# Performance work log

Measured on AMD Instinct MI355X. Metric: run time of the kernel, lower is better.

## Reference

```python
import jax, jax.numpy as jnp
import numpy as np

NC, ND, B, K = 10000, 1000000, 8192, 64
EMB = 16
CH_DENSE, DEV_DENSE = 16, 20
CAT_MAX = [100, 4, 50, 200, 500, 1000, 300]  # lang, plat, os, country, carrier, brand, plat_os
H1, H2, ATTN_H = 64, 64, 84
IN1 = CH_DENSE + EMB        # 32  (channel dense + channel_id emb)
IN2 = DEV_DENSE + 7 * EMB   # 132 (device dense + 7 cat embs)


def setup_inputs() -> dict:
    key = jax.random.key(0)
    ks = jax.random.split(key, 32)
    def nrm(k, shape, s=0.05):
        return jax.random.normal(k, shape, dtype=jnp.float32) * s
    inp = {}
    inp["channel_dense"] = nrm(ks[0], (NC, CH_DENSE), 1.0)
    inp["device_dense"] = nrm(ks[1], (ND, DEV_DENSE), 1.0)
    inp["channel_id_emb"] = nrm(ks[2], (NC, EMB))
    names = ["lang_emb", "plat_emb", "os_emb", "country_emb", "carrier_emb", "brand_emb", "plat_os_emb"]
    for i, (n, m) in enumerate(zip(names, CAT_MAX)):
        inp[n] = nrm(ks[3 + i], (m, EMB))
    inp["W_agg"] = nrm(ks[10], (IN2, H2));  inp["b_agg"] = jnp.zeros((H2,), jnp.float32)
    inp["W_self"] = nrm(ks[11], (IN1, H1)); inp["b_self"] = jnp.zeros((H1,), jnp.float32)
    inp["W_attn"] = nrm(ks[12], (H2 + IN1, ATTN_H)); inp["b_attn"] = jnp.zeros((ATTN_H,), jnp.float32)
    inp["W_attn2"] = nrm(ks[13], (ATTN_H, 1)); inp["b_attn2"] = jnp.zeros((1,), jnp.float32)
    inp["channel_ids"] = jax.random.randint(ks[14], (NC,), 0, NC)
    cat_cols = [jax.random.randint(ks[15 + i], (ND,), 0, m) for i, m in enumerate(CAT_MAX)]
    inp["device_cat"] = jnp.stack(cat_cols, axis=1)  # [ND, 7]
    inp["vertices"] = jax.random.randint(ks[22], (B,), 0, NC)
    inp["bot_neibrs"] = jax.random.randint(ks[23], (B, K), 0, ND)
    inp["normal_neibrs"] = jax.random.randint(ks[24], (B, K), 0, ND)
    inp["bot_counts"] = jax.random.randint(ks[25], (B,), 1, K + 1)
    inp["normal_counts"] = jax.random.randint(ks[26], (B,), 1, K + 1)
    return inp


def reference(channel_dense, device_dense, channel_id_emb, lang_emb, plat_emb, os_emb,
              country_emb, carrier_emb, brand_emb, plat_os_emb,
              W_agg, b_agg, W_self, b_self, W_attn, b_attn, W_attn2, b_attn2,
              channel_ids, device_cat, vertices, bot_neibrs, normal_neibrs,
              bot_counts, normal_counts):
    cat_tables = [lang_emb, plat_emb, os_emb, country_emb, carrier_emb, brand_emb, plat_os_emb]
    # channel self features: dense cols + channel_id embedding  -> [B, IN1]
    ch_v = jnp.concatenate([channel_dense[vertices],
                            channel_id_emb[channel_ids[vertices]]], axis=1)

    def agg(neibrs, counts):
        # gather neighbor device features, embed categoricals, masked mean, linear (Mean_agg)
        dense = device_dense[neibrs]                                   # [B, K, DEV_DENSE]
        cats = device_cat[neibrs]                                      # [B, K, 7]
        embs = jnp.concatenate([t[cats[..., i]] for i, t in enumerate(cat_tables)], axis=-1)
        feats = jnp.concatenate([dense, embs], axis=-1)                # [B, K, IN2]
        mask = (jnp.arange(K)[None, :] < counts[:, None]).astype(feats.dtype)
        mean = jnp.sum(feats * mask[..., None], axis=1) / jnp.maximum(counts, 1).astype(feats.dtype)[:, None]
        return mean @ W_agg + b_agg                                    # [B, H2]

    bots = agg(bot_neibrs, bot_counts)
    normal = agg(normal_neibrs, normal_counts)

    def score(h):
        # attention MLP on concat(aggregated feats, channel self feats)
        return jax.nn.relu(jnp.concatenate([h, ch_v], axis=1) @ W_attn + b_attn) @ W_attn2 + b_attn2

    a = jax.nn.softmax(jnp.concatenate([score(bots), score(normal)], axis=1), axis=1)  # [B, 2]
    gcn = a[:, 0:1] * bots + a[:, 1:2] * normal                        # convex combination [B, H2]
    # Msg_out: relu(concat(agg_out, linear(self)))
    return jax.nn.relu(jnp.concatenate([gcn, ch_v @ W_self + b_self], axis=1))  # [B, H2+H1]
```

## Files before the change

kernel.cpp:

```cpp
#include <hip/hip_runtime.h>

#define BATCH 8192
#define KNB   64
#define EMB   16
#define CHD   16
#define DVD   20
#define H1    64
#define H2    64
#define AH    84
#define IN1   32
#define IN2   132

#define RB 32
#define VB 16
#define NIW 4

typedef float vf4 __attribute__((ext_vector_type(4)));

__global__ __launch_bounds__(128, 4) void gconv_gather(
    const float* __restrict__ device_dense,
    const float* __restrict__ t0, const float* __restrict__ t1,
    const float* __restrict__ t2, const float* __restrict__ t3,
    const float* __restrict__ t4, const float* __restrict__ t5,
    const float* __restrict__ t6,
    const int* __restrict__ device_cat,
    const int* __restrict__ bot_neibrs,
    const int* __restrict__ normal_neibrs,
    const int* __restrict__ bot_counts,
    const int* __restrict__ normal_counts,
    float* __restrict__ fsum_ws)
{
    const int t    = threadIdx.x;
    const int w    = t >> 6;
    const int L    = t & 63;
    const int kk   = L >> 5;
    const int slot = L & 31;

    __shared__ alignas(16) float lds_tab[2464];
    __shared__ alignas(16) int   ofs[2][2][KNB][8];

    for (int i = t; i < 616; i += 128) {
        float4 vsrc;
        if (i < 400)      vsrc = ((const float4*)t0)[i];
        else if (i < 416) vsrc = ((const float4*)t1)[i - 400];
        else              vsrc = ((const float4*)t2)[i - 416];
        ((float4*)lds_tab)[i] = vsrc;
    }

    const int base = (blockIdx.x * 2 + w) * NIW;

    int cnts[NIW];
    #pragma unroll
    for (int i = 0; i < NIW; ++i) {
        const int itn = base + i;
        int c = (itn & 1) ? normal_counts[itn >> 1] : bot_counts[itn >> 1];
        cnts[i] = c < 1 ? 1 : (c > KNB ? KNB : c);
    }

    {
        const int itn = base;
        const int* nbp = (itn & 1) ? normal_neibrs : bot_neibrs;
        const int n = (L < cnts[0]) ? nbp[(itn >> 1) * KNB + L] : 0;
        const long cb = (long)n * 7;
        const int4 cA = *(const int4*)(device_cat + cb);
        const int4 cB = *(const int4*)(device_cat + cb + 3);
        *(int4*)&ofs[w][0][L][0] = make_int4(n * DVD, cA.x * EMB,
                                             1600 + cA.y * EMB, 1664 + cA.z * EMB);
        *(int4*)&ofs[w][0][L][4] = make_int4(cA.w * EMB, cB.y * EMB,
                                             cB.z * EMB, cB.w * EMB);
    }
    __syncthreads();

    const float* P = device_dense;
    int oIdx, col, feat;
    if (slot < 5)       { P = device_dense; oIdx = 0; col = 4 * slot;        feat = col; }
    else if (slot < 9)  { P = t3; oIdx = 4; col = 4 * (slot - 5);  feat = 68  + col; }
    else if (slot < 13) { P = t4; oIdx = 5; col = 4 * (slot - 9);  feat = 84  + col; }
    else if (slot < 17) { P = t5; oIdx = 6; col = 4 * (slot - 13); feat = 100 + col; }
    else if (slot < 21) { P = t6; oIdx = 7; col = 4 * (slot - 17); feat = 116 + col; }
    else if (slot < 25) { oIdx = 1; col = 4 * (slot - 21); feat = 20 + col; }
    else if (slot < 29) { oIdx = 3; col = 4 * (slot - 25); feat = 52 + col; }
    else                { oIdx = 2; col = 4 * (slot - 29); feat = 36 + col; }
    const bool isG = (slot < 21);

    #pragma unroll
    for (int i = 0; i < NIW; ++i) {
        const int cnt = cnts[i];
        const int buf = i & 1;
        const int item = base + i;

        int nNext = 0;
        if (i + 1 < NIW) {
            const int itn = item + 1;
            const int* nbp = (itn & 1) ? normal_neibrs : bot_neibrs;
            nNext = (L < cnts[i + 1]) ? nbp[(itn >> 1) * KNB + L] : 0;
            __builtin_amdgcn_sched_barrier(0);
        }

        vf4 acc  = {0.f, 0.f, 0.f, 0.f};
        vf4 acc2 = {0.f, 0.f, 0.f, 0.f};
        int4 cA = make_int4(0, 0, 0, 0), cB = make_int4(0, 0, 0, 0);

        const int nchunks = (((cnt + 1) >> 1) + 7) >> 3;
        for (int c = 0; c < nchunks; ++c) {
            const int pc = c * 8;
            int o[8];
            #pragma unroll
            for (int j = 0; j < 8; ++j)
                o[j] = ofs[w][buf][2 * (pc + j) + kk][oIdx];
            if (isG) {
                vf4 val[8];
                #pragma unroll
                for (int j = 0; j < 8; ++j) {
                    const float* ap = P + o[j] + col;
                    asm volatile("global_load_dwordx4 %0, %1, off"
                                 : "=v"(val[j]) : "v"(ap) : "memory");
                }
                asm volatile("s_waitcnt vmcnt(0)" ::: "memory");
                __builtin_amdgcn_sched_barrier(0);
                #pragma unroll
                for (int j = 0; j < 8; ++j) {
                    const float m = (2 * (pc + j) + kk < cnt) ? 1.f : 0.f;
                    acc[0] = fmaf(m, val[j][0], acc[0]);
                    acc[1] = fmaf(m, val[j][1], acc[1]);
                    acc[2] = fmaf(m, val[j][2], acc[2]);
                    acc[3] = fmaf(m, val[j][3], acc[3]);
                }
            } else {
                #pragma unroll
                for (int j = 0; j < 8; ++j) {
                    const float m = (2 * (pc + j) + kk < cnt) ? 1.f : 0.f;
                    const float4 lv = *(const float4*)&lds_tab[o[j] + col];
                    acc[0] = fmaf(m, lv.x, acc[0]);
                    acc[1] = fmaf(m, lv.y, acc[1]);
                    acc[2] = fmaf(m, lv.z, acc[2]);
                    acc[3] = fmaf(m, lv.w, acc[3]);
                    if (slot == 29) {
                        const float4 l2 = *(const float4*)&lds_tab[o[j] + 12];
                        acc2[0] = fmaf(m, l2.x, acc2[0]);
                        acc2[1] = fmaf(m, l2.y, acc2[1]);
                        acc2[2] = fmaf(m, l2.z, acc2[2]);
                        acc2[3] = fmaf(m, l2.w, acc2[3]);
                    }
                }
            }
            if (c == 0 && i + 1 < NIW) {
                const long cb = (long)nNext * 7;
                cA = *(const int4*)(device_cat + cb);
                cB = *(const int4*)(device_cat + cb + 3);
                __builtin_amdgcn_sched_barrier(0);
            }
        }

        acc[0] += __shfl_xor(acc[0], 32, 64);
        acc[1] += __shfl_xor(acc[1], 32, 64);
        acc[2] += __shfl_xor(acc[2], 32, 64);
        acc[3] += __shfl_xor(acc[3], 32, 64);
        if (slot == 29) {
            acc2[0] += __shfl_xor(acc2[0], 32, 64);
            acc2[1] += __shfl_xor(acc2[1], 32, 64);
            acc2[2] += __shfl_xor(acc2[2], 32, 64);
            acc2[3] += __shfl_xor(acc2[3], 32, 64);
        }

        if (L < 32)
            *(float4*)(fsum_ws + (size_t)item * IN2 + feat) =
                make_float4(acc[0], acc[1], acc[2], acc[3]);
        if (L == 29)
            *(float4*)(fsum_ws + (size_t)item * IN2 + 48) =
                make_float4(acc2[0], acc2[1], acc2[2], acc2[3]);

        if (i + 1 < NIW) {
            asm volatile("s_waitcnt vmcnt(0)" ::: "memory");
            *(int4*)&ofs[w][buf ^ 1][L][0] = make_int4(nNext * DVD, cA.x * EMB,
                                                 1600 + cA.y * EMB, 1664 + cA.z * EMB);
            *(int4*)&ofs[w][buf ^ 1][L][4] = make_int4(cA.w * EMB, cB.y * EMB,
                                                 cB.z * EMB, cB.w * EMB);
            asm volatile("s_waitcnt lgkmcnt(0)" ::: "memory");
            __builtin_amdgcn_sched_barrier(0);
        }
    }
}

__global__ __launch_bounds__(256) void gconv_dense(
    const float* __restrict__ channel_dense,
    const float* __restrict__ channel_id_emb,
    const float* __restrict__ W_agg,  const float* __restrict__ b_agg,
    const float* __restrict__ W_self, const float* __restrict__ b_self,
    const float* __restrict__ W_attn, const float* __restrict__ b_attn,
    const float* __restrict__ W_attn2,
    const int* __restrict__ channel_ids,
    const int* __restrict__ vertices,
    const int* __restrict__ bot_counts,
    const int* __restrict__ normal_counts,
    const float* __restrict__ fsum_ws,
    float* __restrict__ out)
{
    const int blk = blockIdx.x;
    const int b0  = blk * RB;
    const int v0  = blk * VB;
    const int t   = threadIdx.x;

    __shared__ alignas(16) float fs[RB][IN2];
    __shared__ alignas(16) float chvs[VB][IN1];
    __shared__ alignas(16) float hs[RB][H2];
    __shared__ float u_lds[AH][RB + 1];
    __shared__ float sarr[RB];
    __shared__ float cinv[RB];

    for (int idx = t; idx < RB * IN2 / 4; idx += 256) {
        const float4 vv = *(const float4*)(fsum_ws + (size_t)b0 * IN2 + idx * 4);
        *(float4*)&((float*)fs)[idx * 4] = vv;
    }
    if (t < RB) {
        const int b = b0 + t;
        const int v = b >> 1;
        int c = (b & 1) ? normal_counts[v] : bot_counts[v];
        c = (c > KNB) ? KNB : ((c < 1) ? 1 : c);
        cinv[t] = 1.0f / (float)c;
    }
    if (t < 128) {
        const int vx = t >> 3, q = t & 7;
        const int vert = vertices[v0 + vx];
        const float* src = (q < 4)
            ? channel_dense  + (size_t)vert * CHD + q * 4
            : channel_id_emb + (size_t)channel_ids[vert] * EMB + (q - 4) * 4;
        *(float4*)&chvs[vx][q * 4] = *(const float4*)src;
    }
    __syncthreads();

    {
        const int w = t >> 6, lane = t & 63;
        const int r0 = w * 8;
        float acc[8] = {0.f, 0.f, 0.f, 0.f, 0.f, 0.f, 0.f, 0.f};
        #pragma unroll 4
        for (int f = 0; f < IN2; ++f) {
            const float wv = W_agg[f * H2 + lane];
            #pragma unroll
            for (int r = 0; r < 8; ++r)
                acc[r] = fmaf(fs[r0 + r][f], wv, acc[r]);
        }
        const float bb = b_agg[lane];
        #pragma unroll
        for (int r = 0; r < 8; ++r)
            hs[r0 + r][lane] = fmaf(acc[r], cinv[r0 + r], bb);
    }
    __syncthreads();

    if (t < 2 * AH) {
        const int rg = (t >= AH) ? 1 : 0;
        const int aa = t - AH * rg;
        const int r0 = rg * 16;
        float acc[16];
        #pragma unroll
        for (int r = 0; r < 16; ++r) acc[r] = 0.f;
        #pragma unroll 2
        for (int f = 0; f < H2; ++f) {
            const float wv = W_attn[f * AH + aa];
            #pragma unroll
            for (int r = 0; r < 16; ++r)
                acc[r] = fmaf(hs[r0 + r][f], wv, acc[r]);
        }
        #pragma unroll 2
        for (int f = 0; f < IN1; ++f) {
            const float wv = W_attn[(H2 + f) * AH + aa];
            #pragma unroll
            for (int r = 0; r < 16; ++r)
                acc[r] = fmaf(chvs[(r0 + r) >> 1][f], wv, acc[r]);
        }
        const float ba = b_attn[aa], w2 = W_attn2[aa];
        #pragma unroll
        for (int r = 0; r < 16; ++r)
            u_lds[aa][r0 + r] = fmaxf(acc[r] + ba, 0.f) * w2;
    }
    __syncthreads();

    if (t < RB) {
        float s = 0.f;
        #pragma unroll 4
        for (int aa = 0; aa < AH; ++aa) s += u_lds[aa][t];
        sarr[t] = s;
    }
    __syncthreads();

    {
        const int vl = t >> 4;
        const int c8 = (t & 15) * 8;
        const float s0 = sarr[2 * vl], s1 = sarr[2 * vl + 1];
        const float mm = fmaxf(s0, s1);
        const float e0 = __expf(s0 - mm), e1 = __expf(s1 - mm);
        const float rs = 1.0f / (e0 + e1);
        const float a0 = e0 * rs, a1 = e1 * rs;
        float o[8];
        if (c8 < H2) {
            #pragma unroll
            for (int c = 0; c < 8; ++c)
                o[c] = fmaxf(a0 * hs[2 * vl][c8 + c] + a1 * hs[2 * vl + 1][c8 + c], 0.f);
        } else {
            const int cs = c8 - H2;
            float accS[8];
            #pragma unroll
            for (int c = 0; c < 8; ++c) accS[c] = b_self[cs + c];
            #pragma unroll 4
            for (int f = 0; f < IN1; ++f) {
                const float xv = chvs[vl][f];
                const float4 wa = *(const float4*)(W_self + f * H1 + cs);
                const float4 wb = *(const float4*)(W_self + f * H1 + cs + 4);
                accS[0] = fmaf(xv, wa.x, accS[0]);
                accS[1] = fmaf(xv, wa.y, accS[1]);
                accS[2] = fmaf(xv, wa.z, accS[2]);
                accS[3] = fmaf(xv, wa.w, accS[3]);
                accS[4] = fmaf(xv, wb.x, accS[4]);
                accS[5] = fmaf(xv, wb.y, accS[5]);
                accS[6] = fmaf(xv, wb.z, accS[6]);
                accS[7] = fmaf(xv, wb.w, accS[7]);
            }
            #pragma unroll
            for (int c = 0; c < 8; ++c) o[c] = fmaxf(accS[c], 0.f);
        }
        float4* op = (float4*)(out + (size_t)(v0 + vl) * (H1 + H2) + c8);
        op[0] = make_float4(o[0], o[1], o[2], o[3]);
        op[1] = make_float4(o[4], o[5], o[6], o[7]);
    }
}

extern "C" void kernel_launch(void* const* d_in, const int* in_sizes, int n_in,
                              void* d_out, int out_size, void* d_ws, size_t ws_size,
                              hipStream_t stream) {
    const float* channel_dense  = (const float*)d_in[0];
    const float* device_dense   = (const float*)d_in[1];
    const float* channel_id_emb = (const float*)d_in[2];
    const float* lang_emb       = (const float*)d_in[3];
    const float* plat_emb       = (const float*)d_in[4];
    const float* os_emb         = (const float*)d_in[5];
    const float* country_emb    = (const float*)d_in[6];
    const float* carrier_emb    = (const float*)d_in[7];
    const float* brand_emb      = (const float*)d_in[8];
    const float* plat_os_emb    = (const float*)d_in[9];
    const float* W_agg          = (const float*)d_in[10];
    const float* b_agg          = (const float*)d_in[11];
    const float* W_self         = (const float*)d_in[12];
    const float* b_self         = (const float*)d_in[13];
    const float* W_attn         = (const float*)d_in[14];
    const float* b_attn         = (const float*)d_in[15];
    const float* W_attn2        = (const float*)d_in[16];
    const int* channel_ids   = (const int*)d_in[18];
    const int* device_cat    = (const int*)d_in[19];
    const int* vertices      = (const int*)d_in[20];
    const int* bot_neibrs    = (const int*)d_in[21];
    const int* normal_neibrs = (const int*)d_in[22];
    const int* bot_counts    = (const int*)d_in[23];
    const int* normal_counts = (const int*)d_in[24];

    float* fsum_ws = (float*)d_ws;
    float* out     = (float*)d_out;

    gconv_gather<<<dim3(2 * BATCH / (2 * NIW)), dim3(128), 0, stream>>>(
        device_dense, lang_emb, plat_emb, os_emb, country_emb, carrier_emb,
        brand_emb, plat_os_emb, device_cat, bot_neibrs, normal_neibrs,
        bot_counts, normal_counts, fsum_ws);

    gconv_dense<<<dim3(2 * BATCH / RB), dim3(256), 0, stream>>>(
        channel_dense, channel_id_emb, W_agg, b_agg, W_self, b_self,
        W_attn, b_attn, W_attn2, channel_ids, vertices,
        bot_counts, normal_counts, fsum_ws, out);
}
```

Measured before the change: 75.90 us.

## Process one item per wave in gather kernel, dropping software-pipelined multi-item loop

```diff
diff --git a/kernel.cpp b/kernel.cpp
--- a/kernel.cpp
+++ b/kernel.cpp
@@ -13,11 +13,10 @@
 
 #define RB 32
 #define VB 16
-#define NIW 4
 
 typedef float vf4 __attribute__((ext_vector_type(4)));
 
-__global__ __launch_bounds__(128, 4) void gconv_gather(
+__global__ __launch_bounds__(256, 6) void gconv_gather(
     const float* __restrict__ device_dense,
     const float* __restrict__ t0, const float* __restrict__ t1,
     const float* __restrict__ t2, const float* __restrict__ t3,
@@ -35,11 +34,13 @@
     const int L    = t & 63;
     const int kk   = L >> 5;
     const int slot = L & 31;
+    const int item = blockIdx.x * 4 + w;
+    const int v    = item >> 1;
 
     __shared__ alignas(16) float lds_tab[2464];
-    __shared__ alignas(16) int   ofs[2][2][KNB][8];
-
-    for (int i = t; i < 616; i += 128) {
+    __shared__ alignas(16) int   ofs[4][KNB][8];
+
+    for (int i = t; i < 616; i += 256) {
         float4 vsrc;
         if (i < 400)      vsrc = ((const float4*)t0)[i];
         else if (i < 416) vsrc = ((const float4*)t1)[i - 400];
@@ -47,33 +48,27 @@
         ((float4*)lds_tab)[i] = vsrc;
     }
 
-    const int base = (blockIdx.x * 2 + w) * NIW;
-
-    int cnts[NIW];
-    #pragma unroll
-    for (int i = 0; i < NIW; ++i) {
-        const int itn = base + i;
-        int c = (itn & 1) ? normal_counts[itn >> 1] : bot_counts[itn >> 1];
-        cnts[i] = c < 1 ? 1 : (c > KNB ? KNB : c);
-    }
+    int cnt = (item & 1) ? normal_counts[v] : bot_counts[v];
+    cnt = cnt < 1 ? 1 : (cnt > KNB ? KNB : cnt);
+    cnt = __builtin_amdgcn_readfirstlane(cnt);
 
     {
-        const int itn = base;
-        const int* nbp = (itn & 1) ? normal_neibrs : bot_neibrs;
-        const int n = (L < cnts[0]) ? nbp[(itn >> 1) * KNB + L] : 0;
+        const int* nb = (item & 1) ? normal_neibrs : bot_neibrs;
+        int n = 0;
+        if (L < cnt) n = nb[v * KNB + L];
         const long cb = (long)n * 7;
         const int4 cA = *(const int4*)(device_cat + cb);
         const int4 cB = *(const int4*)(device_cat + cb + 3);
-        *(int4*)&ofs[w][0][L][0] = make_int4(n * DVD, cA.x * EMB,
-                                             1600 + cA.y * EMB, 1664 + cA.z * EMB);
-        *(int4*)&ofs[w][0][L][4] = make_int4(cA.w * EMB, cB.y * EMB,
-                                             cB.z * EMB, cB.w * EMB);
+        *(int4*)&ofs[w][L][0] = make_int4(n * DVD, cA.x * EMB,
+                                          1600 + cA.y * EMB, 1664 + cA.z * EMB);
+        *(int4*)&ofs[w][L][4] = make_int4(cA.w * EMB, cB.y * EMB,
+                                          cB.z * EMB, cB.w * EMB);
     }
     __syncthreads();
 
     const float* P = device_dense;
     int oIdx, col, feat;
-    if (slot < 5)       { P = device_dense; oIdx = 0; col = 4 * slot;        feat = col; }
+    if (slot < 5)       { P = device_dense; oIdx = 0; col = 4 * slot;  feat = col; }
     else if (slot < 9)  { P = t3; oIdx = 4; col = 4 * (slot - 5);  feat = 68  + col; }
     else if (slot < 13) { P = t4; oIdx = 5; col = 4 * (slot - 9);  feat = 84  + col; }
     else if (slot < 17) { P = t5; oIdx = 6; col = 4 * (slot - 13); feat = 100 + col; }
@@ -83,103 +78,69 @@
     else                { oIdx = 2; col = 4 * (slot - 29); feat = 36 + col; }
     const bool isG = (slot < 21);
 
-    #pragma unroll
-    for (int i = 0; i < NIW; ++i) {
-        const int cnt = cnts[i];
-        const int buf = i & 1;
-        const int item = base + i;
-
-        int nNext = 0;
-        if (i + 1 < NIW) {
-            const int itn = item + 1;
-            const int* nbp = (itn & 1) ? normal_neibrs : bot_neibrs;
-            nNext = (L < cnts[i + 1]) ? nbp[(itn >> 1) * KNB + L] : 0;
+    vf4 acc  = {0.f, 0.f, 0.f, 0.f};
+    vf4 acc2 = {0.f, 0.f, 0.f, 0.f};
+    const int passes = (cnt + 1) >> 1;
+    for (int pc = 0; pc < passes; pc += 8) {
+        int o[8];
+        #pragma unroll
+        for (int j = 0; j < 8; ++j)
+            o[j] = ofs[w][2 * (pc + j) + kk][oIdx];
+        if (isG) {
+            vf4 val[8];
+            #pragma unroll
+            for (int j = 0; j < 8; ++j) {
+                const float* ap = P + o[j] + col;
+                asm volatile("global_load_dwordx4 %0, %1, off"
+                             : "=v"(val[j]) : "v"(ap) : "memory");
+            }
+            asm volatile("s_waitcnt vmcnt(0)" ::: "memory");
             __builtin_amdgcn_sched_barrier(0);
-        }
-
-        vf4 acc  = {0.f, 0.f, 0.f, 0.f};
-        vf4 acc2 = {0.f, 0.f, 0.f, 0.f};
-        int4 cA = make_int4(0, 0, 0, 0), cB = make_int4(0, 0, 0, 0);
-
-        const int nchunks = (((cnt + 1) >> 1) + 7) >> 3;
-        for (int c = 0; c < nchunks; ++c) {
-            const int pc = c * 8;
-            int o[8];
-            #pragma unroll
-            for (int j = 0; j < 8; ++j)
-                o[j] = ofs[w][buf][2 * (pc + j) + kk][oIdx];
-            if (isG) {
-                vf4 val[8];
-                #pragma unroll
-                for (int j = 0; j < 8; ++j) {
-                    const float* ap = P + o[j] + col;
-                    asm volatile("global_load_dwordx4 %0, %1, off"
-                                 : "=v"(val[j]) : "v"(ap) : "memory");
-                }
-                asm volatile("s_waitcnt vmcnt(0)" ::: "memory");
-                __builtin_amdgcn_sched_barrier(0);
-                #pragma unroll
-                for (int j = 0; j < 8; ++j) {
-                    const float m = (2 * (pc + j) + kk < cnt) ? 1.f : 0.f;
-                    acc[0] = fmaf(m, val[j][0], acc[0]);
-                    acc[1] = fmaf(m, val[j][1], acc[1]);
-                    acc[2] = fmaf(m, val[j][2], acc[2]);
-                    acc[3] = fmaf(m, val[j][3], acc[3]);
-                }
-            } else {
-                #pragma unroll
-                for (int j = 0; j < 8; ++j) {
-                    const float m = (2 * (pc + j) + kk < cnt) ? 1.f : 0.f;
-                    const float4 lv = *(const float4*)&lds_tab[o[j] + col];
-                    acc[0] = fmaf(m, lv.x, acc[0]);
-                    acc[1] = fmaf(m, lv.y, acc[1]);
-                    acc[2] = fmaf(m, lv.z, acc[2]);
-                    acc[3] = fmaf(m, lv.w, acc[3]);
-                    if (slot == 29) {
-                        const float4 l2 = *(const float4*)&lds_tab[o[j] + 12];
-                        acc2[0] = fmaf(m, l2.x, acc2[0]);
-                        acc2[1] = fmaf(m, l2.y, acc2[1]);
-                        acc2[2] = fmaf(m, l2.z, acc2[2]);
-                        acc2[3] = fmaf(m, l2.w, acc2[3]);
-                    }
+            #pragma unroll
+            for (int j = 0; j < 8; ++j) {
+                const float m = (2 * (pc + j) + kk < cnt) ? 1.f : 0.f;
+                acc[0] = fmaf(m, val[j][0], acc[0]);
+                acc[1] = fmaf(m, val[j][1], acc[1]);
+                acc[2] = fmaf(m, val[j][2], acc[2]);
+                acc[3] = fmaf(m, val[j][3], acc[3]);
+            }
+        } else {
+            #pragma unroll
+            for (int j = 0; j < 8; ++j) {
+                const float m = (2 * (pc + j) + kk < cnt) ? 1.f : 0.f;
+                const float4 lv = *(const float4*)&lds_tab[o[j] + col];
+                acc[0] = fmaf(m, lv.x, acc[0]);
+                acc[1] = fmaf(m, lv.y, acc[1]);
+                acc[2] = fmaf(m, lv.z, acc[2]);
+                acc[3] = fmaf(m, lv.w, acc[3]);
+                if (slot == 29) {
+                    const float4 l2 = *(const float4*)&lds_tab[o[j] + 12];
+                    acc2[0] = fmaf(m, l2.x, acc2[0]);
+                    acc2[1] = fmaf(m, l2.y, acc2[1]);
+                    acc2[2] = fmaf(m, l2.z, acc2[2]);
+                    acc2[3] = fmaf(m, l2.w, acc2[3]);
                 }
             }
-            if (c == 0 && i + 1 < NIW) {
-                const long cb = (long)nNext * 7;
-                cA = *(const int4*)(device_cat + cb);
-                cB = *(const int4*)(device_cat + cb + 3);
-                __builtin_amdgcn_sched_barrier(0);
-            }
-        }
-
-        acc[0] += __shfl_xor(acc[0], 32, 64);
-        acc[1] += __shfl_xor(acc[1], 32, 64);
-        acc[2] += __shfl_xor(acc[2], 32, 64);
-        acc[3] += __shfl_xor(acc[3], 32, 64);
-        if (slot == 29) {
-            acc2[0] += __shfl_xor(acc2[0], 32, 64);
-            acc2[1] += __shfl_xor(acc2[1], 32, 64);
-            acc2[2] += __shfl_xor(acc2[2], 32, 64);
-            acc2[3] += __shfl_xor(acc2[3], 32, 64);
-        }
-
-        if (L < 32)
-            *(float4*)(fsum_ws + (size_t)item * IN2 + feat) =
-                make_float4(acc[0], acc[1], acc[2], acc[3]);
-        if (L == 29)
-            *(float4*)(fsum_ws + (size_t)item * IN2 + 48) =
-                make_float4(acc2[0], acc2[1], acc2[2], acc2[3]);
-
-        if (i + 1 < NIW) {
-            asm volatile("s_waitcnt vmcnt(0)" ::: "memory");
-            *(int4*)&ofs[w][buf ^ 1][L][0] = make_int4(nNext * DVD, cA.x * EMB,
-                                                 1600 + cA.y * EMB, 1664 + cA.z * EMB);
-            *(int4*)&ofs[w][buf ^ 1][L][4] = make_int4(cA.w * EMB, cB.y * EMB,
-                                                 cB.z * EMB, cB.w * EMB);
-            asm volatile("s_waitcnt lgkmcnt(0)" ::: "memory");
-            __builtin_amdgcn_sched_barrier(0);
-        }
-    }
+        }
+    }
+
+    acc[0] += __shfl_xor(acc[0], 32, 64);
+    acc[1] += __shfl_xor(acc[1], 32, 64);
+    acc[2] += __shfl_xor(acc[2], 32, 64);
+    acc[3] += __shfl_xor(acc[3], 32, 64);
+    if (slot == 29) {
+        acc2[0] += __shfl_xor(acc2[0], 32, 64);
+        acc2[1] += __shfl_xor(acc2[1], 32, 64);
+        acc2[2] += __shfl_xor(acc2[2], 32, 64);
+        acc2[3] += __shfl_xor(acc2[3], 32, 64);
+    }
+
+    if (L < 32)
+        *(float4*)(fsum_ws + (size_t)item * IN2 + feat) =
+            make_float4(acc[0], acc[1], acc[2], acc[3]);
+    if (L == 29)
+        *(float4*)(fsum_ws + (size_t)item * IN2 + 48) =
+            make_float4(acc2[0], acc2[1], acc2[2], acc2[3]);
 }
 
 __global__ __launch_bounds__(256) void gconv_dense(
@@ -355,7 +316,7 @@
     float* fsum_ws = (float*)d_ws;
     float* out     = (float*)d_out;
 
-    gconv_gather<<<dim3(2 * BATCH / (2 * NIW)), dim3(128), 0, stream>>>(
+    gconv_gather<<<dim3(2 * BATCH / 4), dim3(256), 0, stream>>>(
         device_dense, lang_emb, plat_emb, os_emb, country_emb, carrier_emb,
         brand_emb, plat_os_emb, device_cat, bot_neibrs, normal_neibrs,
         bot_counts, normal_counts, fsum_ws);
```

Measured after the change: 71.98 us, median of 2. 1.05x faster.
